# Optimization experiments

Hardware: AMD Instinct MI355X
Metric: run time of the kernel (lower is better)

The kernel has to match this reference:

```python
import jax, jax.numpy as jnp
import numpy as np

N_NODES = 20000
N_EDGES = 320000
IN_DIM = 128
HID = 64
HEADS = 4
NEG_SLOPE = 0.2  # PyG GATConv default


def _glorot(key, shape):
    fan_in, fan_out = shape[0], shape[-1]
    lim = jnp.sqrt(6.0 / (fan_in + fan_out))
    return jax.random.uniform(key, shape, jnp.float32, -lim, lim)


def setup_inputs() -> dict:
    key = jax.random.key(0)
    ks = jax.random.split(key, 16)
    x = jax.random.normal(ks[0], (N_NODES, IN_DIM), jnp.float32)
    edge_index = jax.random.randint(ks[1], (2, N_EDGES), 0, N_NODES, dtype=jnp.int64)
    # layer 1: in=128 -> heads=4, out=64, concat
    W1 = _glorot(ks[2], (IN_DIM, HEADS * HID))
    a_src1 = _glorot(ks[3], (HEADS, HID))
    a_dst1 = _glorot(ks[4], (HEADS, HID))
    b1 = jnp.zeros((HEADS * HID,), jnp.float32)
    # layer 2: in=256 -> heads=4, out=64, concat
    W2 = _glorot(ks[5], (HEADS * HID, HEADS * HID))
    a_src2 = _glorot(ks[6], (HEADS, HID))
    a_dst2 = _glorot(ks[7], (HEADS, HID))
    b2 = jnp.zeros((HEADS * HID,), jnp.float32)
    # layer 3: in=256 -> heads=1, out=1, mean (concat=False)
    W3 = _glorot(ks[8], (HEADS * HID, 1))
    a_src3 = _glorot(ks[9], (1, 1))
    a_dst3 = _glorot(ks[10], (1, 1))
    b3 = jnp.zeros((1,), jnp.float32)
    return {
        "x": x, "edge_index": edge_index,
        "W1": W1, "a_src1": a_src1, "a_dst1": a_dst1, "b1": b1,
        "W2": W2, "a_src2": a_src2, "a_dst2": a_dst2, "b2": b2,
        "W3": W3, "a_src3": a_src3, "a_dst3": a_dst3, "b3": b3,
    }


def gat_conv(x, src, dst, W, a_src, a_dst, b, heads, out_c, concat):
    """PyG GATConv (add_self_loops already applied to src/dst)."""
    n = x.shape[0]
    h = (x @ W).reshape(n, heads, out_c)            # [N,H,C]
    alpha_s = jnp.sum(h * a_src, axis=-1)           # [N,H]
    alpha_d = jnp.sum(h * a_dst, axis=-1)           # [N,H]
    e = jax.nn.leaky_relu(alpha_s[src] + alpha_d[dst], NEG_SLOPE)  # [E,H]
    # segment softmax over incoming edges of each destination node
    e_max = jax.ops.segment_max(e, dst, num_segments=n)            # [N,H]
    ex = jnp.exp(e - e_max[dst])                                   # [E,H]
    denom = jax.ops.segment_sum(ex, dst, num_segments=n)           # [N,H]
    alpha = ex / denom[dst]                                        # [E,H]
    msg = h[src] * alpha[:, :, None]                               # [E,H,C]
    out = jax.ops.segment_sum(msg, dst, num_segments=n)            # [N,H,C]
    if concat:
        out = out.reshape(n, heads * out_c)
    else:
        out = out.mean(axis=1)
    return out + b


def reference(x, edge_index, W1, a_src1, a_dst1, b1, W2, a_src2, a_dst2, b2,
              W3, a_src3, a_dst3, b3):
    n = x.shape[0]
    loops = jnp.arange(n, dtype=edge_index.dtype)
    src = jnp.concatenate([edge_index[0], loops])
    dst = jnp.concatenate([edge_index[1], loops])
    h = jax.nn.elu(gat_conv(x, src, dst, W1, a_src1, a_dst1, b1, HEADS, HID, True))
    # dropout is identity in eval mode
    h = jax.nn.elu(gat_conv(h, src, dst, W2, a_src2, a_dst2, b2, HEADS, HID, True))
    h = gat_conv(h, src, dst, W3, a_src3, a_dst3, b3, 1, 1, False)
    return h.reshape(-1)
```

## Files before the change

kernel.cpp:

```cpp
#include <hip/hip_runtime.h>
#include <hip/hip_bf16.h>
#include <cmath>

#define N_NODESC 20000
#define E_RAW    320000
#define E_TOTC   340000
#define HEADSC   4
#define FC       256
#define NEG_SLOPE 0.2f

__device__ __forceinline__ int dstOf(const int* ei, int e) {
  return (e < E_RAW) ? ei[E_RAW + e] : (e - E_RAW);
}
__device__ __forceinline__ int srcOf(const int* ei, int e) {
  return (e < E_RAW) ? ei[e] : (e - E_RAW);
}
__device__ __forceinline__ float lrelu(float v) { return v > 0.f ? v : NEG_SLOPE * v; }

__device__ __forceinline__ unsigned short f2bf(float f) {
  __hip_bfloat16 h = __float2bfloat16(f);
  return reinterpret_cast<unsigned short&>(h);
}
__device__ __forceinline__ float bf2f(unsigned short u) {
  return __uint_as_float(((unsigned int)u) << 16);
}

template<int K>
__global__ void gemm_kernel(const float* __restrict__ A, const float* __restrict__ W,
                            const float* __restrict__ a_src, const float* __restrict__ a_dst,
                            unsigned short* __restrict__ hb, float* __restrict__ as,
                            float* __restrict__ ad) {
  __shared__ float xs[16][K];
  const int t  = threadIdx.x;
  const int m  = t & 63;
  const int rg = t >> 6;
  const int n0 = blockIdx.x * 16;
  for (int idx = t; idx < 16 * (K / 4); idx += 256) {
    int r = idx / (K / 4), c4 = idx - r * (K / 4);
    ((float4*)&xs[r][0])[c4] = ((const float4*)(A + (long)(n0 + r) * K))[c4];
  }
  __syncthreads();
  float4 acc[4];
#pragma unroll
  for (int i = 0; i < 4; ++i) acc[i] = float4{0.f, 0.f, 0.f, 0.f};
  const float* wbase = W + 4 * m;
  for (int k0 = 0; k0 < K; k0 += 4) {
    float4 w0 = *(const float4*)(wbase + (long)(k0 + 0) * FC);
    float4 w1 = *(const float4*)(wbase + (long)(k0 + 1) * FC);
    float4 w2 = *(const float4*)(wbase + (long)(k0 + 2) * FC);
    float4 w3 = *(const float4*)(wbase + (long)(k0 + 3) * FC);
#pragma unroll
    for (int i = 0; i < 4; ++i) {
      float4 a = *(const float4*)&xs[rg * 4 + i][k0];
      acc[i].x = fmaf(a.x, w0.x, acc[i].x); acc[i].y = fmaf(a.x, w0.y, acc[i].y);
      acc[i].z = fmaf(a.x, w0.z, acc[i].z); acc[i].w = fmaf(a.x, w0.w, acc[i].w);
      acc[i].x = fmaf(a.y, w1.x, acc[i].x); acc[i].y = fmaf(a.y, w1.y, acc[i].y);
      acc[i].z = fmaf(a.y, w1.z, acc[i].z); acc[i].w = fmaf(a.y, w1.w, acc[i].w);
      acc[i].x = fmaf(a.z, w2.x, acc[i].x); acc[i].y = fmaf(a.z, w2.y, acc[i].y);
      acc[i].z = fmaf(a.z, w2.z, acc[i].z); acc[i].w = fmaf(a.z, w2.w, acc[i].w);
      acc[i].x = fmaf(a.w, w3.x, acc[i].x); acc[i].y = fmaf(a.w, w3.y, acc[i].y);
      acc[i].z = fmaf(a.w, w3.z, acc[i].z); acc[i].w = fmaf(a.w, w3.w, acc[i].w);
    }
  }
  const int cc = 4 * m;
  const int h  = m >> 4;
  float4 asv = *(const float4*)(a_src + cc);
  float4 adv = *(const float4*)(a_dst + cc);
#pragma unroll
  for (int i = 0; i < 4; ++i) {
    int n = n0 + rg * 4 + i;
    ushort4 pk;
    pk.x = f2bf(acc[i].x); pk.y = f2bf(acc[i].y);
    pk.z = f2bf(acc[i].z); pk.w = f2bf(acc[i].w);
    *(ushort4*)(hb + (long)n * FC + cc) = pk;
    float ps = acc[i].x * asv.x + acc[i].y * asv.y + acc[i].z * asv.z + acc[i].w * asv.w;
    float pd = acc[i].x * adv.x + acc[i].y * adv.y + acc[i].z * adv.z + acc[i].w * adv.w;
    for (int off = 8; off; off >>= 1) {
      ps += __shfl_down(ps, off, 16);
      pd += __shfl_down(pd, off, 16);
    }
    if ((m & 15) == 0) {
      as[n * HEADSC + h] = ps;
      ad[n * HEADSC + h] = pd;
    }
  }
}

__global__ void gemm3_kernel(const float* __restrict__ A, const float* __restrict__ W3,
                             const float* __restrict__ asc, const float* __restrict__ adc,
                             float* __restrict__ h3, float* __restrict__ as,
                             float* __restrict__ ad) {
  const int n = blockIdx.x;
  const int t = threadIdx.x;
  float v = A[(long)n * FC + t] * W3[t];
  for (int off = 32; off; off >>= 1) v += __shfl_down(v, off, 64);
  __shared__ float red[4];
  if ((t & 63) == 0) red[t >> 6] = v;
  __syncthreads();
  if (t == 0) {
    float s = red[0] + red[1] + red[2] + red[3];
    h3[n] = s;
    as[n] = s * asc[0];
    ad[n] = s * adc[0];
  }
}

__global__ void zero_deg(int* __restrict__ deg) {
  int i = blockIdx.x * 256 + threadIdx.x;
  if (i < N_NODESC) deg[i] = 0;
}

__global__ void deg_count(const int* __restrict__ ei, int* __restrict__ deg) {
  int e = blockIdx.x * 256 + threadIdx.x;
  if (e >= E_TOTC) return;
  atomicAdd(&deg[dstOf(ei, e)], 1);
}

__global__ void scan_kernel(const int* __restrict__ deg, int* __restrict__ row_ptr,
                            int* __restrict__ cursor) {
  __shared__ int partial[1024];
  const int t = threadIdx.x;
  const int PER = (N_NODESC + 1023) / 1024;
  const int base = t * PER;
  int s = 0;
  for (int i = 0; i < PER; ++i) {
    int idx = base + i;
    if (idx < N_NODESC) s += deg[idx];
  }
  partial[t] = s;
  __syncthreads();
  for (int off = 1; off < 1024; off <<= 1) {
    int v = (t >= off) ? partial[t - off] : 0;
    __syncthreads();
    partial[t] += v;
    __syncthreads();
  }
  int run = (t == 0) ? 0 : partial[t - 1];
  for (int i = 0; i < PER; ++i) {
    int idx = base + i;
    if (idx < N_NODESC) {
      row_ptr[idx] = run;
      cursor[idx]  = run;
      run += deg[idx];
    }
  }
  if (t == 1023) row_ptr[N_NODESC] = run;
}

__global__ void fill_kernel(const int* __restrict__ ei, int* __restrict__ cursor,
                            int* __restrict__ col_src) {
  int e = blockIdx.x * 256 + threadIdx.x;
  if (e >= E_TOTC) return;
  int d = dstOf(ei, e);
  int pos = atomicAdd(&cursor[d], 1);
  col_src[pos] = srcOf(ei, e);
}

__global__ void softmax4_kernel(const int* __restrict__ row_ptr, const int* __restrict__ col_src,
                                const float4* __restrict__ as4, const float4* __restrict__ ad4,
                                float4* __restrict__ ebuf4, float4* __restrict__ denom4) {
  const int w = threadIdx.x >> 6, l = threadIdx.x & 63;
  const int n = blockIdx.x * 4 + w;
  if (n >= N_NODESC) return;
  const int j0 = row_ptr[n], j1 = row_ptr[n + 1];
  const float4 adv = ad4[n];
  float4 mx = float4{-INFINITY, -INFINITY, -INFINITY, -INFINITY};
  for (int j = j0 + l; j < j1; j += 64) {
    float4 a = as4[col_src[j]];
    float4 v;
    v.x = lrelu(a.x + adv.x); v.y = lrelu(a.y + adv.y);
    v.z = lrelu(a.z + adv.z); v.w = lrelu(a.w + adv.w);
    ebuf4[j] = v;
    mx.x = fmaxf(mx.x, v.x); mx.y = fmaxf(mx.y, v.y);
    mx.z = fmaxf(mx.z, v.z); mx.w = fmaxf(mx.w, v.w);
  }
  for (int off = 32; off; off >>= 1) {
    mx.x = fmaxf(mx.x, __shfl_xor(mx.x, off, 64));
    mx.y = fmaxf(mx.y, __shfl_xor(mx.y, off, 64));
    mx.z = fmaxf(mx.z, __shfl_xor(mx.z, off, 64));
    mx.w = fmaxf(mx.w, __shfl_xor(mx.w, off, 64));
  }
  float4 sm = float4{0.f, 0.f, 0.f, 0.f};
  for (int j = j0 + l; j < j1; j += 64) {
    float4 v = ebuf4[j];
    float4 e;
    e.x = expf(v.x - mx.x); e.y = expf(v.y - mx.y);
    e.z = expf(v.z - mx.z); e.w = expf(v.w - mx.w);
    ebuf4[j] = e;
    sm.x += e.x; sm.y += e.y; sm.z += e.z; sm.w += e.w;
  }
  for (int off = 32; off; off >>= 1) {
    sm.x += __shfl_xor(sm.x, off, 64);
    sm.y += __shfl_xor(sm.y, off, 64);
    sm.z += __shfl_xor(sm.z, off, 64);
    sm.w += __shfl_xor(sm.w, off, 64);
  }
  if (l == 0)
    denom4[n] = float4{1.f / sm.x, 1.f / sm.y, 1.f / sm.z, 1.f / sm.w};
}

__global__ void softmax1_kernel(const int* __restrict__ row_ptr, const int* __restrict__ col_src,
                                const float* __restrict__ as, const float* __restrict__ ad,
                                float* __restrict__ ebuf, float* __restrict__ denom) {
  const int w = threadIdx.x >> 6, l = threadIdx.x & 63;
  const int n = blockIdx.x * 4 + w;
  if (n >= N_NODESC) return;
  const int j0 = row_ptr[n], j1 = row_ptr[n + 1];
  const float adv = ad[n];
  float mx = -INFINITY;
  for (int j = j0 + l; j < j1; j += 64) {
    float v = lrelu(as[col_src[j]] + adv);
    ebuf[j] = v;
    mx = fmaxf(mx, v);
  }
  for (int off = 32; off; off >>= 1) mx = fmaxf(mx, __shfl_xor(mx, off, 64));
  float sm = 0.f;
  for (int j = j0 + l; j < j1; j += 64) {
    float e = expf(ebuf[j] - mx);
    ebuf[j] = e;
    sm += e;
  }
  for (int off = 32; off; off >>= 1) sm += __shfl_xor(sm, off, 64);
  if (l == 0) denom[n] = 1.f / sm;
}

template<bool ELU>
__global__ void agg_kernel(const int* __restrict__ row_ptr, const int* __restrict__ col_src,
                           const float* __restrict__ ebuf, const float* __restrict__ denom,
                           const unsigned short* __restrict__ hb, const float* __restrict__ b,
                           float* __restrict__ outbuf) {
  const int d = blockIdx.x;
  const int t = threadIdx.x;
  const int h = t >> 5;
  const int j0 = row_ptr[d], j1 = row_ptr[d + 1];
  const ushort2* hb2 = (const ushort2*)hb;
  float a0 = 0.f, a1 = 0.f;
  int j = j0;
  for (; j + 8 <= j1; j += 8) {
    int     s[8];
    ushort2 v[8];
    float   w[8];
#pragma unroll
    for (int u = 0; u < 8; ++u) s[u] = col_src[j + u];
#pragma unroll
    for (int u = 0; u < 8; ++u) v[u] = hb2[(long)s[u] * 128 + t];
#pragma unroll
    for (int u = 0; u < 8; ++u) w[u] = ebuf[(j + u) * HEADSC + h];
#pragma unroll
    for (int u = 0; u < 8; ++u) {
      a0 = fmaf(w[u], bf2f(v[u].x), a0);
      a1 = fmaf(w[u], bf2f(v[u].y), a1);
    }
  }
  for (; j < j1; ++j) {
    ushort2 v = hb2[(long)col_src[j] * 128 + t];
    float w = ebuf[j * HEADSC + h];
    a0 = fmaf(w, bf2f(v.x), a0);
    a1 = fmaf(w, bf2f(v.y), a1);
  }
  float dn = denom[d * HEADSC + h];
  float o0 = a0 * dn + b[2 * t];
  float o1 = a1 * dn + b[2 * t + 1];
  if (ELU) {
    o0 = o0 > 0.f ? o0 : expm1f(o0);
    o1 = o1 > 0.f ? o1 : expm1f(o1);
  }
  *(float2*)(outbuf + (long)d * FC + 2 * t) = float2{o0, o1};
}

__global__ void agg3_kernel(const int* __restrict__ row_ptr, const int* __restrict__ col_src,
                            const float* __restrict__ ebuf, const float* __restrict__ denom,
                            const float* __restrict__ h3, const float* __restrict__ b3,
                            float* __restrict__ out) {
  const int wv = threadIdx.x >> 6;
  const int l  = threadIdx.x & 63;
  const int d  = blockIdx.x * 4 + wv;
  if (d >= N_NODESC) return;
  const int j0 = row_ptr[d], j1 = row_ptr[d + 1];
  float acc = 0.f;
  for (int j = j0 + l; j < j1; j += 64)
    acc = fmaf(ebuf[j], h3[col_src[j]], acc);
  for (int off = 32; off; off >>= 1) acc += __shfl_down(acc, off, 64);
  if (l == 0) out[d] = acc * denom[d] + b3[0];
}

extern "C" void kernel_launch(void* const* d_in, const int* in_sizes, int n_in,
                              void* d_out, int out_size, void* d_ws, size_t ws_size,
                              hipStream_t stream) {
  const float* x    = (const float*)d_in[0];
  const int*   ei   = (const int*)d_in[1];
  const float* W1   = (const float*)d_in[2];
  const float* as1  = (const float*)d_in[3];
  const float* ad1  = (const float*)d_in[4];
  const float* b1   = (const float*)d_in[5];
  const float* W2   = (const float*)d_in[6];
  const float* as2  = (const float*)d_in[7];
  const float* ad2  = (const float*)d_in[8];
  const float* b2   = (const float*)d_in[9];
  const float* W3   = (const float*)d_in[10];
  const float* as3  = (const float*)d_in[11];
  const float* ad3  = (const float*)d_in[12];
  const float* b3   = (const float*)d_in[13];
  float* out = (float*)d_out;

  float* ws    = (float*)d_ws;
  float*         act = ws;
  unsigned short* hb = (unsigned short*)(act + (size_t)N_NODESC * FC);
  float* wAs   = act + (size_t)N_NODESC * FC + (size_t)N_NODESC * FC / 2;
  float* wAd   = wAs   + (size_t)N_NODESC * HEADSC;
  float* denom = wAd   + (size_t)N_NODESC * HEADSC;
  float* ebuf  = denom + (size_t)N_NODESC * HEADSC;
  float* h3    = ebuf  + (size_t)E_TOTC * HEADSC;
  int*   ibase = (int*)(h3 + N_NODESC);
  int*   deg     = ibase;
  int*   row_ptr = deg + N_NODESC;
  int*   cursor  = row_ptr + N_NODESC + 1;
  int*   col_src = cursor + N_NODESC;

  const int gridE  = (E_TOTC + 255) / 256;
  const int gridN  = (N_NODESC + 255) / 256;
  const int gridN4 = (N_NODESC + 3) / 4;
  const int gemmG  = N_NODESC / 16;

  zero_deg<<<gridN, 256, 0, stream>>>(deg);
  deg_count<<<gridE, 256, 0, stream>>>(ei, deg);
  scan_kernel<<<1, 1024, 0, stream>>>(deg, row_ptr, cursor);
  fill_kernel<<<gridE, 256, 0, stream>>>(ei, cursor, col_src);

  gemm_kernel<128><<<gemmG, 256, 0, stream>>>(x, W1, as1, ad1, hb, wAs, wAd);
  softmax4_kernel<<<gridN4, 256, 0, stream>>>(row_ptr, col_src, (const float4*)wAs,
                                              (const float4*)wAd, (float4*)ebuf, (float4*)denom);
  agg_kernel<true><<<N_NODESC, 128, 0, stream>>>(row_ptr, col_src, ebuf, denom, hb, b1, act);

  gemm_kernel<256><<<gemmG, 256, 0, stream>>>(act, W2, as2, ad2, hb, wAs, wAd);
  softmax4_kernel<<<gridN4, 256, 0, stream>>>(row_ptr, col_src, (const float4*)wAs,
                                              (const float4*)wAd, (float4*)ebuf, (float4*)denom);
  agg_kernel<true><<<N_NODESC, 128, 0, stream>>>(row_ptr, col_src, ebuf, denom, hb, b2, act);

  gemm3_kernel<<<N_NODESC, 256, 0, stream>>>(act, W3, as3, ad3, h3, wAs, wAd);
  softmax1_kernel<<<gridN4, 256, 0, stream>>>(row_ptr, col_src, wAs, wAd, ebuf, denom);
  agg3_kernel<<<gridN4, 256, 0, stream>>>(row_ptr, col_src, ebuf, denom, h3, b3, out);
}
```

Baseline: 255.9 us.

## Split GEMM K dimension across warps and reduce partial sums in shared memory

The node-feature GEMM now gives each of the four wavefronts a quarter of the K range across all 16 rows, instead of 4 rows over the full K. Each weight float4 loaded from global memory is then reused for 16 rows rather than 4, which cuts weight traffic per block fourfold. The partial sums are combined serially through a 16x256 shared buffer with four barriers. This raises register pressure to 64 accumulators per thread and adds 16 KB of shared memory, which may lower occupancy.

```diff
diff --git a/kernel.cpp b/kernel.cpp
--- a/kernel.cpp
+++ b/kernel.cpp
@@ -31,50 +31,92 @@
                             unsigned short* __restrict__ hb, float* __restrict__ as,
                             float* __restrict__ ad) {
   __shared__ float xs[16][K];
+  __shared__ float red[16][FC];
   const int t  = threadIdx.x;
   const int m  = t & 63;
-  const int rg = t >> 6;
+  const int w  = t >> 6;
   const int n0 = blockIdx.x * 16;
+
   for (int idx = t; idx < 16 * (K / 4); idx += 256) {
     int r = idx / (K / 4), c4 = idx - r * (K / 4);
     ((float4*)&xs[r][0])[c4] = ((const float4*)(A + (long)(n0 + r) * K))[c4];
   }
   __syncthreads();
-  float4 acc[4];
-#pragma unroll
-  for (int i = 0; i < 4; ++i) acc[i] = float4{0.f, 0.f, 0.f, 0.f};
+
+  float4 acc[16];
+#pragma unroll
+  for (int r = 0; r < 16; ++r) acc[r] = float4{0.f, 0.f, 0.f, 0.f};
+
   const float* wbase = W + 4 * m;
-  for (int k0 = 0; k0 < K; k0 += 4) {
+  const int kbeg = w * (K / 4), kend = kbeg + (K / 4);
+  for (int k0 = kbeg; k0 < kend; k0 += 4) {
     float4 w0 = *(const float4*)(wbase + (long)(k0 + 0) * FC);
     float4 w1 = *(const float4*)(wbase + (long)(k0 + 1) * FC);
     float4 w2 = *(const float4*)(wbase + (long)(k0 + 2) * FC);
     float4 w3 = *(const float4*)(wbase + (long)(k0 + 3) * FC);
 #pragma unroll
-    for (int i = 0; i < 4; ++i) {
-      float4 a = *(const float4*)&xs[rg * 4 + i][k0];
-      acc[i].x = fmaf(a.x, w0.x, acc[i].x); acc[i].y = fmaf(a.x, w0.y, acc[i].y);
-      acc[i].z = fmaf(a.x, w0.z, acc[i].z); acc[i].w = fmaf(a.x, w0.w, acc[i].w);
-      acc[i].x = fmaf(a.y, w1.x, acc[i].x); acc[i].y = fmaf(a.y, w1.y, acc[i].y);
-      acc[i].z = fmaf(a.y, w1.z, acc[i].z); acc[i].w = fmaf(a.y, w1.w, acc[i].w);
-      acc[i].x = fmaf(a.z, w2.x, acc[i].x); acc[i].y = fmaf(a.z, w2.y, acc[i].y);
-      acc[i].z = fmaf(a.z, w2.z, acc[i].z); acc[i].w = fmaf(a.z, w2.w, acc[i].w);
-      acc[i].x = fmaf(a.w, w3.x, acc[i].x); acc[i].y = fmaf(a.w, w3.y, acc[i].y);
-      acc[i].z = fmaf(a.w, w3.z, acc[i].z); acc[i].w = fmaf(a.w, w3.w, acc[i].w);
-    }
-  }
+    for (int r = 0; r < 16; ++r) {
+      float4 a = ((const float4*)&xs[r][0])[k0 >> 2];
+      acc[r].x = fmaf(a.x, w0.x, acc[r].x); acc[r].y = fmaf(a.x, w0.y, acc[r].y);
+      acc[r].z = fmaf(a.x, w0.z, acc[r].z); acc[r].w = fmaf(a.x, w0.w, acc[r].w);
+      acc[r].x = fmaf(a.y, w1.x, acc[r].x); acc[r].y = fmaf(a.y, w1.y, acc[r].y);
+      acc[r].z = fmaf(a.y, w1.z, acc[r].z); acc[r].w = fmaf(a.y, w1.w, acc[r].w);
+      acc[r].x = fmaf(a.z, w2.x, acc[r].x); acc[r].y = fmaf(a.z, w2.y, acc[r].y);
+      acc[r].z = fmaf(a.z, w2.z, acc[r].z); acc[r].w = fmaf(a.z, w2.w, acc[r].w);
+      acc[r].x = fmaf(a.w, w3.x, acc[r].x); acc[r].y = fmaf(a.w, w3.y, acc[r].y);
+      acc[r].z = fmaf(a.w, w3.z, acc[r].z); acc[r].w = fmaf(a.w, w3.w, acc[r].w);
+    }
+  }
+
+  float4* red4row;
+  if (w == 0) {
+#pragma unroll
+    for (int r = 0; r < 16; ++r) ((float4*)&red[r][0])[m] = acc[r];
+  }
+  __syncthreads();
+  if (w == 1) {
+#pragma unroll
+    for (int r = 0; r < 16; ++r) {
+      float4 v = ((float4*)&red[r][0])[m];
+      v.x += acc[r].x; v.y += acc[r].y; v.z += acc[r].z; v.w += acc[r].w;
+      ((float4*)&red[r][0])[m] = v;
+    }
+  }
+  __syncthreads();
+  if (w == 2) {
+#pragma unroll
+    for (int r = 0; r < 16; ++r) {
+      float4 v = ((float4*)&red[r][0])[m];
+      v.x += acc[r].x; v.y += acc[r].y; v.z += acc[r].z; v.w += acc[r].w;
+      ((float4*)&red[r][0])[m] = v;
+    }
+  }
+  __syncthreads();
+  if (w == 3) {
+#pragma unroll
+    for (int r = 0; r < 16; ++r) {
+      float4 v = ((float4*)&red[r][0])[m];
+      v.x += acc[r].x; v.y += acc[r].y; v.z += acc[r].z; v.w += acc[r].w;
+      ((float4*)&red[r][0])[m] = v;
+    }
+  }
+  __syncthreads();
+
   const int cc = 4 * m;
   const int h  = m >> 4;
   float4 asv = *(const float4*)(a_src + cc);
   float4 adv = *(const float4*)(a_dst + cc);
 #pragma unroll
   for (int i = 0; i < 4; ++i) {
-    int n = n0 + rg * 4 + i;
+    int r = w * 4 + i;
+    int n = n0 + r;
+    float4 v = ((float4*)&red[r][0])[m];
     ushort4 pk;
-    pk.x = f2bf(acc[i].x); pk.y = f2bf(acc[i].y);
-    pk.z = f2bf(acc[i].z); pk.w = f2bf(acc[i].w);
+    pk.x = f2bf(v.x); pk.y = f2bf(v.y);
+    pk.z = f2bf(v.z); pk.w = f2bf(v.w);
     *(ushort4*)(hb + (long)n * FC + cc) = pk;
-    float ps = acc[i].x * asv.x + acc[i].y * asv.y + acc[i].z * asv.z + acc[i].w * asv.w;
-    float pd = acc[i].x * adv.x + acc[i].y * adv.y + acc[i].z * adv.z + acc[i].w * adv.w;
+    float ps = v.x * asv.x + v.y * asv.y + v.z * asv.z + v.w * asv.w;
+    float pd = v.x * adv.x + v.y * adv.y + v.z * adv.z + v.w * adv.w;
     for (int off = 8; off; off >>= 1) {
       ps += __shfl_down(ps, off, 16);
       pd += __shfl_down(pd, off, 16);
```

Measured after the change: 250.6 us. -2.1%, faster.

## Replace FP32 FMA GEMMs with split-bf16 MFMA GEMMs and separate alpha kernel

Applied to the files above, without the earlier changes.

Replaces the scalar fp32 GEMMs for layers 1 and 2 with MFMA 16x16x32 bf16 matrix instructions. Precision is kept near fp32 by splitting each operand into hi and lo bf16 parts and issuing three MFMAs per tile (hi*hi, hi*lo, lo*hi). Activations are now written as hi/lo bf16 pairs by the aggregation kernel. Weights are transposed and split each call, and x is split up front. The attention logit computation moves out of the GEMM epilogue into a separate alpha kernel that rereads the bf16 features, which adds launches and extra memory traffic.

```diff
diff --git a/kernel.cpp b/kernel.cpp
--- a/kernel.cpp
+++ b/kernel.cpp
@@ -9,6 +9,9 @@
 #define FC       256
 #define NEG_SLOPE 0.2f
 
+typedef __attribute__((ext_vector_type(8))) short short8v;
+typedef __attribute__((ext_vector_type(4))) float f32x4;
+
 __device__ __forceinline__ int dstOf(const int* ei, int e) {
   return (e < E_RAW) ? ei[E_RAW + e] : (e - E_RAW);
 }
@@ -25,74 +28,96 @@
   return __uint_as_float(((unsigned int)u) << 16);
 }
 
+__global__ void prep_split(const float* __restrict__ in, unsigned short* __restrict__ hi,
+                           unsigned short* __restrict__ lo, int n) {
+  int i = blockIdx.x * 256 + threadIdx.x;
+  if (i >= n) return;
+  float v = in[i];
+  unsigned short h = f2bf(v);
+  hi[i] = h;
+  lo[i] = f2bf(v - bf2f(h));
+}
+
 template<int K>
-__global__ void gemm_kernel(const float* __restrict__ A, const float* __restrict__ W,
-                            const float* __restrict__ a_src, const float* __restrict__ a_dst,
-                            unsigned short* __restrict__ hb, float* __restrict__ as,
-                            float* __restrict__ ad) {
-  __shared__ float xs[16][K];
-  const int t  = threadIdx.x;
-  const int m  = t & 63;
-  const int rg = t >> 6;
+__global__ void prep_wt(const float* __restrict__ W, unsigned short* __restrict__ hiT,
+                        unsigned short* __restrict__ loT) {
+  int idx = blockIdx.x * 256 + threadIdx.x;
+  if (idx >= 256 * K) return;
+  int c = idx / K, k = idx - c * K;
+  float v = W[(long)k * FC + c];
+  unsigned short h = f2bf(v);
+  hiT[(long)c * K + k] = h;
+  loT[(long)c * K + k] = f2bf(v - bf2f(h));
+}
+
+template<int K>
+__global__ void __launch_bounds__(256) mfma_gemm(
+    const unsigned short* __restrict__ Ahi, const unsigned short* __restrict__ Alo,
+    const unsigned short* __restrict__ WhiT, const unsigned short* __restrict__ WloT,
+    unsigned short* __restrict__ hb) {
+  const int t = threadIdx.x;
+  const int w = t >> 6, l = t & 63;
   const int n0 = blockIdx.x * 16;
-  for (int idx = t; idx < 16 * (K / 4); idx += 256) {
-    int r = idx / (K / 4), c4 = idx - r * (K / 4);
-    ((float4*)&xs[r][0])[c4] = ((const float4*)(A + (long)(n0 + r) * K))[c4];
-  }
-  __syncthreads();
-  float4 acc[4];
-#pragma unroll
-  for (int i = 0; i < 4; ++i) acc[i] = float4{0.f, 0.f, 0.f, 0.f};
-  const float* wbase = W + 4 * m;
-  for (int k0 = 0; k0 < K; k0 += 4) {
-    float4 w0 = *(const float4*)(wbase + (long)(k0 + 0) * FC);
-    float4 w1 = *(const float4*)(wbase + (long)(k0 + 1) * FC);
-    float4 w2 = *(const float4*)(wbase + (long)(k0 + 2) * FC);
-    float4 w3 = *(const float4*)(wbase + (long)(k0 + 3) * FC);
-#pragma unroll
-    for (int i = 0; i < 4; ++i) {
-      float4 a = *(const float4*)&xs[rg * 4 + i][k0];
-      acc[i].x = fmaf(a.x, w0.x, acc[i].x); acc[i].y = fmaf(a.x, w0.y, acc[i].y);
-      acc[i].z = fmaf(a.x, w0.z, acc[i].z); acc[i].w = fmaf(a.x, w0.w, acc[i].w);
-      acc[i].x = fmaf(a.y, w1.x, acc[i].x); acc[i].y = fmaf(a.y, w1.y, acc[i].y);
-      acc[i].z = fmaf(a.y, w1.z, acc[i].z); acc[i].w = fmaf(a.y, w1.w, acc[i].w);
-      acc[i].x = fmaf(a.z, w2.x, acc[i].x); acc[i].y = fmaf(a.z, w2.y, acc[i].y);
-      acc[i].z = fmaf(a.z, w2.z, acc[i].z); acc[i].w = fmaf(a.z, w2.w, acc[i].w);
-      acc[i].x = fmaf(a.w, w3.x, acc[i].x); acc[i].y = fmaf(a.w, w3.y, acc[i].y);
-      acc[i].z = fmaf(a.w, w3.z, acc[i].z); acc[i].w = fmaf(a.w, w3.w, acc[i].w);
+  const int r16 = l & 15;
+  const int kq = l >> 4;
+  const int col0 = w * 64;
+  f32x4 acc[4];
+#pragma unroll
+  for (int ct = 0; ct < 4; ++ct) acc[ct] = f32x4{0.f, 0.f, 0.f, 0.f};
+  const long arow = (long)(n0 + r16) * K;
+  for (int ks = 0; ks < K; ks += 32) {
+    const int kb = ks + kq * 8;
+    short8v aHi = *(const short8v*)(Ahi + arow + kb);
+    short8v aLo = *(const short8v*)(Alo + arow + kb);
+#pragma unroll
+    for (int ct = 0; ct < 4; ++ct) {
+      const long wrow = (long)(col0 + ct * 16 + r16) * K + kb;
+      short8v wHi = *(const short8v*)(WhiT + wrow);
+      short8v wLo = *(const short8v*)(WloT + wrow);
+      acc[ct] = __builtin_amdgcn_mfma_f32_16x16x32_bf16(aHi, wHi, acc[ct], 0, 0, 0);
+      acc[ct] = __builtin_amdgcn_mfma_f32_16x16x32_bf16(aHi, wLo, acc[ct], 0, 0, 0);
+      acc[ct] = __builtin_amdgcn_mfma_f32_16x16x32_bf16(aLo, wHi, acc[ct], 0, 0, 0);
     }
   }
-  const int cc = 4 * m;
-  const int h  = m >> 4;
-  float4 asv = *(const float4*)(a_src + cc);
-  float4 adv = *(const float4*)(a_dst + cc);
-#pragma unroll
-  for (int i = 0; i < 4; ++i) {
-    int n = n0 + rg * 4 + i;
-    ushort4 pk;
-    pk.x = f2bf(acc[i].x); pk.y = f2bf(acc[i].y);
-    pk.z = f2bf(acc[i].z); pk.w = f2bf(acc[i].w);
-    *(ushort4*)(hb + (long)n * FC + cc) = pk;
-    float ps = acc[i].x * asv.x + acc[i].y * asv.y + acc[i].z * asv.z + acc[i].w * asv.w;
-    float pd = acc[i].x * adv.x + acc[i].y * adv.y + acc[i].z * adv.z + acc[i].w * adv.w;
-    for (int off = 8; off; off >>= 1) {
-      ps += __shfl_down(ps, off, 16);
-      pd += __shfl_down(pd, off, 16);
+#pragma unroll
+  for (int ct = 0; ct < 4; ++ct) {
+    int c = col0 + ct * 16 + r16;
+#pragma unroll
+    for (int j = 0; j < 4; ++j) {
+      int r = n0 + kq * 4 + j;
+      hb[(long)r * FC + c] = f2bf(acc[ct][j]);
     }
-    if ((m & 15) == 0) {
-      as[n * HEADSC + h] = ps;
-      ad[n * HEADSC + h] = pd;
-    }
-  }
-}
-
-__global__ void gemm3_kernel(const float* __restrict__ A, const float* __restrict__ W3,
+  }
+}
+
+__global__ void alpha_kernel(const unsigned short* __restrict__ hb,
+                             const float* __restrict__ a_src, const float* __restrict__ a_dst,
+                             float* __restrict__ as, float* __restrict__ ad) {
+  const int n = blockIdx.x;
+  const int t = threadIdx.x;
+  float hv = bf2f(hb[(long)n * FC + t]);
+  float vs = hv * a_src[t];
+  float vd = hv * a_dst[t];
+  for (int off = 32; off; off >>= 1) {
+    vs += __shfl_down(vs, off, 64);
+    vd += __shfl_down(vd, off, 64);
+  }
+  if ((t & 63) == 0) {
+    as[n * HEADSC + (t >> 6)] = vs;
+    ad[n * HEADSC + (t >> 6)] = vd;
+  }
+}
+
+__global__ void gemm3_kernel(const unsigned short* __restrict__ act_hi,
+                             const unsigned short* __restrict__ act_lo,
+                             const float* __restrict__ W3,
                              const float* __restrict__ asc, const float* __restrict__ adc,
                              float* __restrict__ h3, float* __restrict__ as,
                              float* __restrict__ ad) {
   const int n = blockIdx.x;
   const int t = threadIdx.x;
-  float v = A[(long)n * FC + t] * W3[t];
+  float a = bf2f(act_hi[(long)n * FC + t]) + bf2f(act_lo[(long)n * FC + t]);
+  float v = a * W3[t];
   for (int off = 32; off; off >>= 1) v += __shfl_down(v, off, 64);
   __shared__ float red[4];
   if ((t & 63) == 0) red[t >> 6] = v;
@@ -228,7 +253,7 @@
 __global__ void agg_kernel(const int* __restrict__ row_ptr, const int* __restrict__ col_src,
                            const float* __restrict__ ebuf, const float* __restrict__ denom,
                            const unsigned short* __restrict__ hb, const float* __restrict__ b,
-                           float* __restrict__ outbuf) {
+                           unsigned short* __restrict__ out_hi, unsigned short* __restrict__ out_lo) {
   const int d = blockIdx.x;
   const int t = threadIdx.x;
   const int h = t >> 5;
@@ -265,7 +290,11 @@
     o0 = o0 > 0.f ? o0 : expm1f(o0);
     o1 = o1 > 0.f ? o1 : expm1f(o1);
   }
-  *(float2*)(outbuf + (long)d * FC + 2 * t) = float2{o0, o1};
+  ushort2 hi, lo;
+  hi.x = f2bf(o0); lo.x = f2bf(o0 - bf2f(hi.x));
+  hi.y = f2bf(o1); lo.y = f2bf(o1 - bf2f(hi.y));
+  ((ushort2*)out_hi)[(long)d * 128 + t] = hi;
+  ((ushort2*)out_lo)[(long)d * 128 + t] = lo;
 }
 
 __global__ void agg3_kernel(const int* __restrict__ row_ptr, const int* __restrict__ col_src,
@@ -303,19 +332,25 @@
   const float* b3   = (const float*)d_in[13];
   float* out = (float*)d_out;
 
-  float* ws    = (float*)d_ws;
-  float*         act = ws;
-  unsigned short* hb = (unsigned short*)(act + (size_t)N_NODESC * FC);
-  float* wAs   = act + (size_t)N_NODESC * FC + (size_t)N_NODESC * FC / 2;
-  float* wAd   = wAs   + (size_t)N_NODESC * HEADSC;
-  float* denom = wAd   + (size_t)N_NODESC * HEADSC;
-  float* ebuf  = denom + (size_t)N_NODESC * HEADSC;
-  float* h3    = ebuf  + (size_t)E_TOTC * HEADSC;
-  int*   ibase = (int*)(h3 + N_NODESC);
-  int*   deg     = ibase;
-  int*   row_ptr = deg + N_NODESC;
-  int*   cursor  = row_ptr + N_NODESC + 1;
-  int*   col_src = cursor + N_NODESC;
+  float* ws = (float*)d_ws;
+  size_t off = 0;
+  float* wAs   = ws + off; off += (size_t)N_NODESC * HEADSC;
+  float* wAd   = ws + off; off += (size_t)N_NODESC * HEADSC;
+  float* denom = ws + off; off += (size_t)N_NODESC * HEADSC;
+  float* ebuf  = ws + off; off += (size_t)E_TOTC * HEADSC;
+  float* h3    = ws + off; off += N_NODESC;
+  int* deg     = (int*)(ws + off); off += N_NODESC;
+  int* row_ptr = (int*)(ws + off); off += N_NODESC + 1;
+  int* cursor  = (int*)(ws + off); off += N_NODESC;
+  int* col_src = (int*)(ws + off); off += E_TOTC;
+  off = (off + 3) & ~(size_t)3;
+  unsigned short* hb     = (unsigned short*)(ws + off); off += (size_t)N_NODESC * 128;
+  unsigned short* act_hi = (unsigned short*)(ws + off); off += (size_t)N_NODESC * 128;
+  unsigned short* act_lo = (unsigned short*)(ws + off); off += (size_t)N_NODESC * 128;
+  unsigned short* xhi    = (unsigned short*)(ws + off); off += (size_t)N_NODESC * 64;
+  unsigned short* xlo    = (unsigned short*)(ws + off); off += (size_t)N_NODESC * 64;
+  unsigned short* WhiT   = (unsigned short*)(ws + off); off += 32768;
+  unsigned short* WloT   = (unsigned short*)(ws + off); off += 32768;
 
   const int gridE  = (E_TOTC + 255) / 256;
   const int gridN  = (N_NODESC + 255) / 256;
@@ -326,18 +361,25 @@
   deg_count<<<gridE, 256, 0, stream>>>(ei, deg);
   scan_kernel<<<1, 1024, 0, stream>>>(deg, row_ptr, cursor);
   fill_kernel<<<gridE, 256, 0, stream>>>(ei, cursor, col_src);
-
-  gemm_kernel<128><<<gemmG, 256, 0, stream>>>(x, W1, as1, ad1, hb, wAs, wAd);
+  prep_split<<<(N_NODESC * 128 + 255) / 256, 256, 0, stream>>>(x, xhi, xlo, N_NODESC * 128);
+
+  prep_wt<128><<<(256 * 128 + 255) / 256, 256, 0, stream>>>(W1, WhiT, WloT);
+  mfma_gemm<128><<<gemmG, 256, 0, stream>>>(xhi, xlo, WhiT, WloT, hb);
+  alpha_kernel<<<N_NODESC, 256, 0, stream>>>(hb, as1, ad1, wAs, wAd);
   softmax4_kernel<<<gridN4, 256, 0, stream>>>(row_ptr, col_src, (const float4*)wAs,
                                               (const float4*)wAd, (float4*)ebuf, (float4*)denom);
-  agg_kernel<true><<<N_NODESC, 128, 0, stream>>>(row_ptr, col_src, ebuf, denom, hb, b1, act);
-
-  gemm_kernel<256><<<gemmG, 256, 0, stream>>>(act, W2, as2, ad2, hb, wAs, wAd);
+  agg_kernel<true><<<N_NODESC, 128, 0, stream>>>(row_ptr, col_src, ebuf, denom, hb, b1,
+                                                 act_hi, act_lo);
+
+  prep_wt<256><<<(256 * 256 + 255) / 256, 256, 0, stream>>>(W2, WhiT, WloT);
+  mfma_gemm<256><<<gemmG, 256, 0, stream>>>(act_hi, act_lo, WhiT, WloT, hb);
+  alpha_kernel<<<N_NODESC, 256, 0, stream>>>(hb, as2, ad2, wAs, wAd);
   softmax4_kernel<<<gridN4, 256, 0, stream>>>(row_ptr, col_src, (const float4*)wAs,
                                               (const float4*)wAd, (float4*)ebuf, (float4*)denom);
-  agg_kernel<true><<<N_NODESC, 128, 0, stream>>>(row_ptr, col_src, ebuf, denom, hb, b2, act);
-
-  gemm3_kernel<<<N_NODESC, 256, 0, stream>>>(act, W3, as3, ad3, h3, wAs, wAd);
+  agg_kernel<true><<<N_NODESC, 128, 0, stream>>>(row_ptr, col_src, ebuf, denom, hb, b2,
+                                                 act_hi, act_lo);
+
+  gemm3_kernel<<<N_NODESC, 256, 0, stream>>>(act_hi, act_lo, W3, as3, ad3, h3, wAs, wAd);
   softmax1_kernel<<<gridN4, 256, 0, stream>>>(row_ptr, col_src, wAs, wAd, ebuf, denom);
   agg3_kernel<<<gridN4, 256, 0, stream>>>(row_ptr, col_src, ebuf, denom, h3, b3, out);
 }
```

After: 297.5 us. +16.3%, slower.
